# Performance work log

Measured on AMD Instinct MI355X. Metric: run time of the kernel, lower is better.

## Reference

```python
import jax, jax.numpy as jnp
import numpy as np

LEAKY = 0.1  # leaky_hmm_coefficient (pychain default)


def _fb_objf(x_exp, tfrom, tto, tpdf, tprob, init_p, final_p):
    """Leaky-HMM forward recursion for one sequence.
    x_exp: [T, P] exp'd nnet outputs; transitions are edge lists of length E.
    Returns scalar log-prob of the sequence under the graph.
    """
    S = init_p.shape[0]

    def step(carry, obs):
        alpha, logz = carry  # alpha: [S] normalized occupation probs
        # per-edge contribution: alpha[src] * trans_prob * obs[pdf]
        contrib = alpha[tfrom] * tprob * obs[tpdf]          # [E]
        new_alpha = jnp.zeros(S, alpha.dtype).at[tto].add(contrib)
        tot = new_alpha.sum()
        # leaky-HMM: redistribute a fraction of total mass via initial probs
        new_alpha = new_alpha + LEAKY * tot * init_p
        scale = new_alpha.sum()
        return (new_alpha / scale, logz + jnp.log(scale)), None

    (alpha_T, logz), _ = jax.lax.scan(step, (init_p, jnp.zeros((), x_exp.dtype)), x_exp)
    return logz + jnp.log(jnp.sum(alpha_T * final_p))


def setup_inputs() -> dict:
    key = jax.random.key(0)
    ks = jax.random.split(key, 12)
    B, T, P = 32, 500, 3000
    S_den, E_den = 2000, 40000
    S_num, E_num = 100, 400

    x = jax.random.normal(ks[0], (B, T, P), jnp.float32)

    # denominator graph (shared across batch); every state gets incoming arcs
    den_to = (jnp.arange(E_den, dtype=jnp.int32) % S_den)
    den_from = jax.random.randint(ks[1], (E_den,), 0, S_den, jnp.int32)
    den_pdf = jax.random.randint(ks[2], (E_den,), 0, P, jnp.int32)
    den_prob = jax.random.uniform(ks[3], (E_den,), jnp.float32, 0.1, 1.0)
    den_init = jax.random.uniform(ks[4], (S_den,), jnp.float32, 0.1, 1.0)
    den_init = den_init / den_init.sum()
    den_final = jax.random.uniform(ks[5], (S_den,), jnp.float32, 0.1, 1.0)

    # numerator graphs (one per utterance), batched edge lists
    num_to = jnp.tile(jnp.arange(E_num, dtype=jnp.int32) % S_num, (B, 1))
    num_from = jax.random.randint(ks[6], (B, E_num), 0, S_num, jnp.int32)
    num_pdf = jax.random.randint(ks[7], (B, E_num), 0, P, jnp.int32)
    num_prob = jax.random.uniform(ks[8], (B, E_num), jnp.float32, 0.1, 1.0)
    num_init = jax.random.uniform(ks[9], (B, S_num), jnp.float32, 0.1, 1.0)
    num_init = num_init / num_init.sum(axis=1, keepdims=True)
    num_final = jax.random.uniform(ks[10], (B, S_num), jnp.float32, 0.1, 1.0)

    return {
        "x": x,
        "den_from": den_from, "den_to": den_to, "den_pdf": den_pdf,
        "den_prob": den_prob, "den_init": den_init, "den_final": den_final,
        "num_from": num_from, "num_to": num_to, "num_pdf": num_pdf,
        "num_prob": num_prob, "num_init": num_init, "num_final": num_final,
    }


def reference(x, den_from, den_to, den_pdf, den_prob, den_init, den_final,
              num_from, num_to, num_pdf, num_prob, num_init, num_final):
    B, T, _ = x.shape
    exp_x = jnp.exp(jnp.clip(x, -30.0, 30.0))  # [B, T, P]

    # denominator: shared graph across batch
    den_objf = jax.vmap(_fb_objf, in_axes=(0, None, None, None, None, None, None))(
        exp_x, den_from, den_to, den_pdf, den_prob, den_init, den_final).sum()
    # numerator: per-utterance graph
    num_objf = jax.vmap(_fb_objf, in_axes=(0, 0, 0, 0, 0, 0, 0))(
        exp_x, num_from, num_to, num_pdf, num_prob, num_init, num_final).sum()

    objf = -(num_objf - den_objf)
    return objf / (B * T)  # avg=True
```

## Files before the change

kernel.cpp:

```cpp
#include <hip/hip_runtime.h>


#define LEAKY 0.1f
#define AGENT __HIP_MEMORY_SCOPE_AGENT

constexpr int B = 32, T = 500, P = 3000;
constexpr int S_DEN = 2000;
constexpr int S_NUM = 100, E_NUM = 400;
constexpr int NTH = 1024;
constexpr int NWAVE = NTH / 64;
constexpr int G_DEN = 5;
constexpr int SB = S_DEN / G_DEN;
constexpr int KE = 20;
constexpr int EPT = KE / 2;
constexpr int OBS_T0 = 800;
constexpr int OBS_N = NTH - OBS_T0;
constexpr int OBS_IT = (P + OBS_N - 1) / OBS_N;
constexpr int KE_NUM = 4;
constexpr int NDEN_BLK = B * G_DEN;


__device__ __forceinline__ float clampexp(float x) {
  return __expf(fminf(fmaxf(x, -30.f), 30.f));
}
__device__ __forceinline__ void st_f32(float* p, float v) {
  __hip_atomic_store(p, v, __ATOMIC_RELAXED, AGENT);
}
__device__ __forceinline__ unsigned long long ld_u64(const float* p) {
  return __hip_atomic_load((const unsigned long long*)p, __ATOMIC_RELAXED,
                           AGENT);
}

template <int CTRL, int RMASK, bool BC>
__device__ __forceinline__ float dpp_add(float v) {
  const int s =
      __builtin_amdgcn_update_dpp(0, __float_as_int(v), CTRL, RMASK, 0xf, BC);
  return v + __int_as_float(s);
}
__device__ __forceinline__ float dpp_xor1_add(float v) {
  const int s =
      __builtin_amdgcn_update_dpp(0, __float_as_int(v), 0xB1, 0xf, 0xf, true);
  return v + __int_as_float(s);
}
__device__ __forceinline__ float wave_sum63(float v) {
  v = dpp_add<0x111, 0xf, true>(v);
  v = dpp_add<0x112, 0xf, true>(v);
  v = dpp_add<0x114, 0xf, true>(v);
  v = dpp_add<0x118, 0xf, true>(v);
  v = dpp_add<0x142, 0xa, false>(v);
  v = dpp_add<0x143, 0xc, false>(v);
  return v;
}

__device__ __forceinline__ float reduce_1024(float v, float* wpart) {
#pragma unroll
  for (int off = 32; off; off >>= 1) v += __shfl_xor(v, off, 64);
  if ((threadIdx.x & 63) == 0) wpart[threadIdx.x >> 6] = v;
  __syncthreads();
  float s = 0.f;
#pragma unroll
  for (int w = 0; w < NWAVE; ++w) s += wpart[w];
  return s;
}

__device__ void run_den(const float* __restrict__ xb,
                        const int* __restrict__ ef_g,
                        const int* __restrict__ ep_g,
                        const float* __restrict__ epr_g,
                        const float* __restrict__ einit,
                        const float* __restrict__ efinal, int b, int g,
                        float* __restrict__ outs, float* __restrict__ parts_b,
                        float* obsA, float* obsB, float* cur, float* ini_s,
                        float* wpart) {
  const int tid = threadIdx.x;
  const int lane = tid & 63;
  const bool gat = tid < 2 * SB;
  const bool cons = tid < S_DEN / 2;
  const int jloc = (tid >> 6) * 32 + (lane >> 1);
  const int half = lane & 1;
  const int j = g * SB + jloc;

  float lsum = 0.f;
  if (cons) {
    const float2 iv = ((const float2*)einit)[tid];
    ((float2*)ini_s)[tid] = iv;
    lsum = iv.x + iv.y;
  }
  __syncthreads();
  const float leakfac = 1.f + LEAKY * reduce_1024(lsum, wpart);

  int efep[EPT];
  float epr[EPT], w[EPT], c[EPT];
  if (gat) {
#pragma unroll
    for (int k = 0; k < EPT; ++k) {
      const int e = j + (half * EPT + k) * S_DEN;
      efep[k] = ef_g[e] | (ep_g[e] << 16);
      epr[k] = epr_g[e];
    }
    const int off = (3 * lane) & 31;
#pragma unroll
    for (int i = 0; i < EPT - 1; ++i) {
#pragma unroll
      for (int k = 0; k < EPT - 1 - i; ++k) {
        const int ka = ((efep[k] & 31) - off) & 31;
        const int kb = ((efep[k + 1] & 31) - off) & 31;
        if (kb < ka) {
          const int te = efep[k]; efep[k] = efep[k + 1]; efep[k + 1] = te;
          const float tp = epr[k]; epr[k] = epr[k + 1]; epr[k + 1] = tp;
        }
      }
    }
#pragma unroll
    for (int k = 0; k < EPT; ++k) c[k] = ini_s[efep[k] & 0xffff] * epr[k];
  }

  obsA[tid] = clampexp(xb[tid]);
  obsA[tid + 1024] = clampexp(xb[tid + 1024]);
  if (tid + 2048 < P) obsA[tid + 2048] = clampexp(xb[tid + 2048]);
  float xr[OBS_IT];
  if (tid >= OBS_T0) {
    const float* r = xb + P;
#pragma unroll
    for (int i = 0; i < OBS_IT; ++i) {
      const int p = tid - OBS_T0 + OBS_N * i;
      xr[i] = (p < P) ? r[p] : 0.f;
    }
  }
  __syncthreads();
  float iniw = 0.f;
  if (gat) {
#pragma unroll
    for (int k = 0; k < EPT; ++k) {
      const float o = obsA[efep[k] >> 16];
      w[k] = epr[k] * o;
      iniw += c[k] * o;
    }
  }

  float logz = 0.f;
  for (int t = 0; t < T; ++t) {
    float* obs_n = (t & 1) ? obsA : obsB;
    if (tid < 832) __builtin_amdgcn_s_setprio(1);
    float a_raw = 0.f, lt = 0.f, inv = 0.f;
    if (t && gat) {
#pragma unroll
      for (int k = 0; k < EPT; ++k) a_raw += cur[efep[k] & 0xffff] * w[k];
      const float4* wq = (const float4*)wpart;
      const float4 q0 = wq[0], q1 = wq[1], q2 = wq[2], q3 = wq[3];
      float s = q0.x; s += q0.y; s += q0.z; s += q0.w;
      s += q1.x; s += q1.y; s += q1.z; s += q1.w;
      s += q2.x; s += q2.y; s += q2.z; s += q2.w;
      s += q3.x; s += q3.y; s += q3.z; s += q3.w;
      const float scale = s * leakfac;
      lt = LEAKY * s;
      inv = 1.f / scale;
      logz += __logf(scale);
    }
    const int parn = (t + 1) & 1;
    const unsigned tagn = ((unsigned)(t + 1) >> 1) & 1u;
    if (gat) {
      const float ar = dpp_xor1_add(a_raw);
      const float iw = dpp_xor1_add(iniw);
      if (!half) {
        const float aa = t ? inv * fmaf(lt, iw, ar) : iw;
        st_f32(parts_b + parn * 2048 + j, tagn ? -aa : aa);
      }
    } else if (tid >= OBS_T0) {
      float nxr[OBS_IT];
      const int tn = (t + 2 < T) ? t + 2 : T - 1;
      const float* r = xb + (size_t)tn * P;
#pragma unroll
      for (int i = 0; i < OBS_IT; ++i) {
        const int p = tid - OBS_T0 + OBS_N * i;
        nxr[i] = (p < P) ? r[p] : 0.f;
      }
      if (t + 1 < T) {
#pragma unroll
        for (int i = 0; i < OBS_IT; ++i) {
          const int p = tid - OBS_T0 + OBS_N * i;
          if (p < P) obs_n[p] = clampexp(xr[i]);
        }
      }
#pragma unroll
      for (int i = 0; i < OBS_IT; ++i) xr[i] = nxr[i];
    }
    if (tid < 832) __builtin_amdgcn_s_setprio(0);
    __syncthreads();
    const float* myp = parts_b + parn * 2048 + 2 * tid;
    unsigned long long u = 0;
    if (cons) u = ld_u64(myp);
    if (gat && t + 1 < T) {
      iniw = 0.f;
#pragma unroll
      for (int k = 0; k < EPT; ++k) {
        const float o = obs_n[efep[k] >> 16];
        w[k] = epr[k] * o;
        iniw += c[k] * o;
      }
    }
    if (cons) {
      const auto bad = [&](unsigned long long v) {
        return (((unsigned)(v >> 31) & 1u) != tagn) ||
               (((unsigned)(v >> 63) & 1u) != tagn);
      };
      if (bad(u)) u = ld_u64(myp);
      while (bad(u)) {
        __builtin_amdgcn_s_sleep(1);
        u = ld_u64(myp);
      }
    }
    union { unsigned long long q; float2 f; } cc;
    cc.q = u;
    const float2 v2 = make_float2(fabsf(cc.f.x), fabsf(cc.f.y));
    const float pv = wave_sum63(cons ? (v2.x + v2.y) : 0.f);
    if (lane == 63) wpart[tid >> 6] = pv;
    if (cons) ((float2*)cur)[tid] = v2;
    __syncthreads();
  }

  float s = 0.f;
#pragma unroll
  for (int wv = 0; wv < NWAVE; ++wv) s += wpart[wv];
  const float scaleT = s * leakfac;
  logz += __logf(scaleT);
  const float ltT = LEAKY * s, invT = 1.f / scaleT;
  float fv = 0.f;
  if (cons) {
    const float2 f2 = ((const float2*)efinal)[tid];
    const float2 i2 = ((const float2*)ini_s)[tid];
    const float2 c2 = ((const float2*)cur)[tid];
    fv = (fmaf(ltT, i2.x, c2.x) * invT) * f2.x +
         (fmaf(ltT, i2.y, c2.y) * invT) * f2.y;
  }
  __syncthreads();
  const float fin = reduce_1024(fv, wpart);
  if (tid == 0 && g == 0) outs[b] = logz + __logf(fin);
}

__device__ void run_num(const float* __restrict__ xb, const int* __restrict__ ef,
                        const int* __restrict__ ep, const float* __restrict__ epr,
                        const float* __restrict__ einit,
                        const float* __restrict__ efinal,
                        float* __restrict__ out_slot, float* __restrict__ obs,
                        float* __restrict__ cur, float* __restrict__ wpart) {
  const int tid = threadIdx.x;
  const bool act = tid < S_NUM / 2;
  const int j = 2 * tid;
  float2 ini = make_float2(0.f, 0.f), fin2 = make_float2(0.f, 0.f);
  if (act) {
    ini = ((const float2*)einit)[tid];
    fin2 = ((const float2*)efinal)[tid];
  }
  __syncthreads();
  const float leakfac =
      1.f + LEAKY * reduce_1024(act ? ini.x + ini.y : 0.f, wpart);

  int2 f2[KE_NUM], p2[KE_NUM];
  float2 pr2[KE_NUM];
  if (act) {
#pragma unroll
    for (int k = 0; k < KE_NUM; ++k) {
      f2[k] = ((const int2*)(ef + k * S_NUM))[tid];
      p2[k] = ((const int2*)(ep + k * S_NUM))[tid];
      pr2[k] = ((const float2*)(epr + k * S_NUM))[tid];
    }
  }
  obs[tid] = clampexp(xb[tid]);
  obs[tid + 1024] = clampexp(xb[tid + 1024]);
  if (tid + 2048 < P) obs[tid + 2048] = clampexp(xb[tid + 2048]);
  float xr0, xr1, xr2;
  {
    const float* r = xb + P;
    xr0 = r[tid];
    xr1 = r[tid + 1024];
    xr2 = (tid + 2048 < P) ? r[tid + 2048] : 0.f;
  }
  if (act) {
    cur[j] = ini.x;
    cur[j + 1] = ini.y;
  }
  __syncthreads();

  float logz = 0.f;
  for (int t = 0; t < T; ++t) {
    float nx0 = xr0, nx1 = xr1, nx2 = xr2;
    if (t + 2 < T) {
      const float* r = xb + (size_t)(t + 2) * P;
      nx0 = r[tid];
      nx1 = r[tid + 1024];
      nx2 = (tid + 2048 < P) ? r[tid + 2048] : 0.f;
    }
    float a0 = 0.f, a1 = 0.f;
    if (act) {
#pragma unroll
      for (int k = 0; k < KE_NUM; ++k) {
        a0 += cur[f2[k].x] * pr2[k].x * obs[p2[k].x];
        a1 += cur[f2[k].y] * pr2[k].y * obs[p2[k].y];
      }
    }
    float v = a0 + a1;
#pragma unroll
    for (int off = 32; off; off >>= 1) v += __shfl_xor(v, off, 64);
    if ((tid & 63) == 0) wpart[tid >> 6] = v;
    __syncthreads();
    float tot = 0.f;
#pragma unroll
    for (int w = 0; w < NWAVE; ++w) tot += wpart[w];
    if (t + 1 < T) {
      obs[tid] = clampexp(xr0);
      obs[tid + 1024] = clampexp(xr1);
      if (tid + 2048 < P) obs[tid + 2048] = clampexp(xr2);
    }
    xr0 = nx0;
    xr1 = nx1;
    xr2 = nx2;
    const float scale = tot * leakfac;
    const float inv = 1.f / scale, lt = LEAKY * tot;
    if (act) {
      cur[j] = fmaf(lt, ini.x, a0) * inv;
      cur[j + 1] = fmaf(lt, ini.y, a1) * inv;
    }
    logz += __logf(scale);
    __syncthreads();
  }
  __syncthreads();
  const float fin = reduce_1024(
      act ? (cur[j] * fin2.x + cur[j + 1] * fin2.y) : 0.f, wpart);
  if (tid == 0) *out_slot = logz + __logf(fin);
}

__global__ __launch_bounds__(NTH) void fb_kernel(
    const float* __restrict__ x, const int* __restrict__ den_from,
    const int* __restrict__ den_pdf, const float* __restrict__ den_prob,
    const float* __restrict__ den_init, const float* __restrict__ den_final,
    const int* __restrict__ num_from, const int* __restrict__ num_pdf,
    const float* __restrict__ num_prob, const float* __restrict__ num_init,
    const float* __restrict__ num_final, float* __restrict__ ws) {
  __shared__ float obsA[P];
  __shared__ float obsB[P];
  __shared__ float cur[S_DEN];
  __shared__ float ini_s[S_DEN];
  __shared__ float wpart[NWAVE];
  float* outs = ws;
  float* parts = ws + 4096;
  const int blk = blockIdx.x;
  if (blk < NDEN_BLK) {
    const int xcd = blk & 7, m = blk >> 3;
    const int b = (m / 5) * 8 + xcd;
    const int g = m % 5;
    run_den(x + (size_t)b * T * P, den_from, den_pdf, den_prob, den_init,
            den_final, b, g, outs, parts + (size_t)b * 4096, obsA, obsB, cur,
            ini_s, wpart);
  } else {
    const int b = blk - NDEN_BLK;
    run_num(x + (size_t)b * T * P, num_from + b * E_NUM, num_pdf + b * E_NUM,
            num_prob + b * E_NUM, num_init + b * S_NUM, num_final + b * S_NUM,
            outs + B + b, obsA, cur, wpart);
  }
}

__global__ void init_parts(float* p) {
  const int i = blockIdx.x * NTH + threadIdx.x;
  st_f32(&p[i], ((i >> 11) & 1) ? -1.f : 1.f);
}

__global__ void finish_kernel(const float* __restrict__ ws,
                              float* __restrict__ out) {
  const int tid = threadIdx.x;
  float v = ws[tid];
  v = (tid < B) ? v : -v;
#pragma unroll
  for (int off = 32; off; off >>= 1) v += __shfl_xor(v, off, 64);
  if (tid == 0) out[0] = v / (float)(B * T);
}

extern "C" void kernel_launch(void* const* d_in, const int* in_sizes, int n_in,
                              void* d_out, int out_size, void* d_ws,
                              size_t ws_size, hipStream_t stream) {
  const float* x = (const float*)d_in[0];
  const int* den_from = (const int*)d_in[1];
  const int* den_pdf = (const int*)d_in[3];
  const float* den_prob = (const float*)d_in[4];
  const float* den_init = (const float*)d_in[5];
  const float* den_final = (const float*)d_in[6];
  const int* num_from = (const int*)d_in[7];
  const int* num_pdf = (const int*)d_in[9];
  const float* num_prob = (const float*)d_in[10];
  const float* num_init = (const float*)d_in[11];
  const float* num_final = (const float*)d_in[12];
  float* ws = (float*)d_ws;
  float* out = (float*)d_out;

  init_parts<<<(B * 4096) / NTH, NTH, 0, stream>>>(ws + 4096);
  fb_kernel<<<NDEN_BLK + B, NTH, 0, stream>>>(
      x, den_from, den_pdf, den_prob, den_init, den_final, num_from, num_pdf,
      num_prob, num_init, num_final, ws);
  finish_kernel<<<1, 64, 0, stream>>>(ws, out);
}
```

Before: 1.312 ms.

## Gather den alpha directly from global parts buffer instead of LDS copy

Each gather thread now prefetches its source-state alpha values straight from the global cross-block parts buffer (tag-bit checked), and spins per edge if a value is stale, instead of reading them from a shared-memory copy written by the consumer threads. This removes the LDS store of cur and lets the gather loads for step t+1 be issued early, overlapping with the rest of the step. In exchange it adds scattered global atomic loads per edge and extra spin loops, which may raise L2 traffic and latency on the critical path.

Result: slower. 3.058 ms (+133.1%).

```diff
diff --git a/kernel.cpp b/kernel.cpp
--- a/kernel.cpp
+++ b/kernel.cpp
@@ -26,6 +26,9 @@
 __device__ __forceinline__ void st_f32(float* p, float v) {
   __hip_atomic_store(p, v, __ATOMIC_RELAXED, AGENT);
 }
+__device__ __forceinline__ float ld_f32(const float* p) {
+  return __hip_atomic_load(p, __ATOMIC_RELAXED, AGENT);
+}
 __device__ __forceinline__ unsigned long long ld_u64(const float* p) {
   return __hip_atomic_load((const unsigned long long*)p, __ATOMIC_RELAXED,
                            AGENT);
@@ -70,7 +73,7 @@
                         const float* __restrict__ einit,
                         const float* __restrict__ efinal, int b, int g,
                         float* __restrict__ outs, float* __restrict__ parts_b,
-                        float* obsA, float* obsB, float* cur, float* ini_s,
+                        float* obsA, float* obsB, float* ini_s,
                         float* wpart) {
   const int tid = threadIdx.x;
   const int lane = tid & 63;
@@ -90,7 +93,7 @@
   const float leakfac = 1.f + LEAKY * reduce_1024(lsum, wpart);
 
   int efep[EPT];
-  float epr[EPT], w[EPT], c[EPT];
+  float epr[EPT], w[EPT], c[EPT], gv[EPT];
   if (gat) {
 #pragma unroll
     for (int k = 0; k < EPT; ++k) {
@@ -112,7 +115,10 @@
       }
     }
 #pragma unroll
-    for (int k = 0; k < EPT; ++k) c[k] = ini_s[efep[k] & 0xffff] * epr[k];
+    for (int k = 0; k < EPT; ++k) {
+      c[k] = ini_s[efep[k] & 0xffff] * epr[k];
+      gv[k] = 0.f;
+    }
   }
 
   obsA[tid] = clampexp(xb[tid]);
@@ -139,13 +145,21 @@
   }
 
   float logz = 0.f;
+  float2 v2 = make_float2(0.f, 0.f);
   for (int t = 0; t < T; ++t) {
     float* obs_n = (t & 1) ? obsA : obsB;
     if (tid < 832) __builtin_amdgcn_s_setprio(1);
     float a_raw = 0.f, lt = 0.f, inv = 0.f;
     if (t && gat) {
-#pragma unroll
-      for (int k = 0; k < EPT; ++k) a_raw += cur[efep[k] & 0xffff] * w[k];
+      const unsigned tagc = ((unsigned)t >> 1) & 1u;
+      const float* pc = parts_b + (t & 1) * 2048;
+#pragma unroll
+      for (int k = 0; k < EPT; ++k) {
+        float v = gv[k];
+        while ((__float_as_uint(v) >> 31) != tagc)
+          v = ld_f32(pc + (efep[k] & 0xffff));
+        a_raw += fabsf(v) * w[k];
+      }
       const float4* wq = (const float4*)wpart;
       const float4 q0 = wq[0], q1 = wq[1], q2 = wq[2], q3 = wq[3];
       float s = q0.x; s += q0.y; s += q0.z; s += q0.w;
@@ -191,6 +205,11 @@
     unsigned long long u = 0;
     if (cons) u = ld_u64(myp);
     if (gat && t + 1 < T) {
+      const float* pn = parts_b + parn * 2048;
+#pragma unroll
+      for (int k = 0; k < EPT; ++k) gv[k] = ld_f32(pn + (efep[k] & 0xffff));
+    }
+    if (gat && t + 1 < T) {
       iniw = 0.f;
 #pragma unroll
       for (int k = 0; k < EPT; ++k) {
@@ -212,10 +231,9 @@
     }
     union { unsigned long long q; float2 f; } cc;
     cc.q = u;
-    const float2 v2 = make_float2(fabsf(cc.f.x), fabsf(cc.f.y));
+    v2 = make_float2(fabsf(cc.f.x), fabsf(cc.f.y));
     const float pv = wave_sum63(cons ? (v2.x + v2.y) : 0.f);
     if (lane == 63) wpart[tid >> 6] = pv;
-    if (cons) ((float2*)cur)[tid] = v2;
     __syncthreads();
   }
 
@@ -229,9 +247,8 @@
   if (cons) {
     const float2 f2 = ((const float2*)efinal)[tid];
     const float2 i2 = ((const float2*)ini_s)[tid];
-    const float2 c2 = ((const float2*)cur)[tid];
-    fv = (fmaf(ltT, i2.x, c2.x) * invT) * f2.x +
-         (fmaf(ltT, i2.y, c2.y) * invT) * f2.y;
+    fv = (fmaf(ltT, i2.x, v2.x) * invT) * f2.x +
+         (fmaf(ltT, i2.y, v2.y) * invT) * f2.y;
   }
   __syncthreads();
   const float fin = reduce_1024(fv, wpart);
@@ -350,7 +367,7 @@
     const int b = (m / 5) * 8 + xcd;
     const int g = m % 5;
     run_den(x + (size_t)b * T * P, den_from, den_pdf, den_prob, den_init,
-            den_final, b, g, outs, parts + (size_t)b * 4096, obsA, obsB, cur,
+            den_final, b, g, outs, parts + (size_t)b * 4096, obsA, obsB,
             ini_s, wpart);
   } else {
     const int b = blk - NDEN_BLK;
```
